# Kernel tuning notes

Hardware: AMD Instinct MI355X
Metric: run time of the kernel (lower is better)

Reference implementation:

```python
import jax, jax.numpy as jnp
import numpy as np

B, S, D = 2, 2048, 2048
H, KVH, HD = 16, 8, 128          # heads, kv heads, head_dim
KVR = 512                        # kv_lora_rank
THETA, ROPE_FACTOR = 10000.0, 40.0
EPS = 1e-5
NEG = -1e9


def _layernorm(x, scale):
    mean = jnp.mean(x, axis=-1, keepdims=True)
    var = jnp.mean(jnp.square(x - mean), axis=-1, keepdims=True)
    return (x - mean) * jax.lax.rsqrt(var + EPS) * scale


def _rope_cos_sin(position_ids):
    # freqs over half the head dim, scaled by rope_factor (as in source)
    freqs = (1.0 / THETA ** (jnp.arange(0, HD, 2, dtype=jnp.float32) / HD)) * ROPE_FACTOR
    ang = position_ids.astype(jnp.float32)[:, None] * freqs[None, :]  # [S, HD//2]
    return jnp.cos(ang)[None, :, None, :], jnp.sin(ang)[None, :, None, :]


def _apply_rope(x, cos, sin):
    # x: [B,S,h,HD] with interleaved (real, imag) pairs
    x_ = x.reshape(*x.shape[:-1], -1, 2)
    xr, xi = x_[..., 0], x_[..., 1]
    out = jnp.stack([xr * cos - xi * sin, xr * sin + xi * cos], axis=-1)
    return out.reshape(x.shape)


def setup_inputs() -> dict:
    key = jax.random.key(0)
    ks = jax.random.split(key, 6)
    std = 0.02
    x = jax.random.normal(ks[0], (B, S, D), jnp.float32)
    wq = jax.random.normal(ks[1], (D, H * 2 * HD), jnp.float32) * std
    wkv_a = jax.random.normal(ks[2], (D, KVR + HD), jnp.float32) * std
    kv_norm_scale = jnp.ones((KVR,), jnp.float32)
    wkv_b = jax.random.normal(ks[3], (KVR, KVH * 2 * HD), jnp.float32) * std
    wo = jax.random.normal(ks[4], (H * HD, D), jnp.float32) * std
    causal = jnp.tril(jnp.ones((S, S), bool))
    attention_mask = jnp.where(causal, 0.0, NEG)[None, None].astype(jnp.float32)
    position_ids = jnp.arange(S, dtype=jnp.int32)
    return {"x": x, "wq": wq, "wkv_a": wkv_a, "kv_norm_scale": kv_norm_scale,
            "wkv_b": wkv_b, "wo": wo, "attention_mask": attention_mask,
            "position_ids": position_ids}


def reference(x, wq, wkv_a, kv_norm_scale, wkv_b, wo, attention_mask, position_ids):
    cos, sin = _rope_cos_sin(position_ids)
    # Q path: low-rank disabled (q_lora_rank=0) -> single projection
    q = (x @ wq).reshape(B, S, H, 2 * HD)
    q_nope, q_pe = q[..., :HD], q[..., HD:]
    q = jnp.concatenate([q_nope, _apply_rope(q_pe, cos, sin)], axis=-1)  # [B,S,H,2HD]
    # KV path: low-rank compression + decoupled rope key
    kv = x @ wkv_a                               # [B,S,KVR+HD]
    kv_c = _layernorm(kv[..., :KVR], kv_norm_scale)
    k_pe = kv[..., KVR:]                         # [B,S,HD]
    kvb = (kv_c @ wkv_b).reshape(B, S, KVH, 2 * HD)
    k_nope, v = kvb[..., :HD], kvb[..., HD:]
    k_pe = _apply_rope(k_pe[:, :, None, :], cos, sin)  # [B,S,1,HD]
    k = jnp.concatenate([k_nope, jnp.broadcast_to(k_pe, (B, S, KVH, HD))], axis=-1)
    # GQA expansion
    rep = H // KVH
    k = jnp.repeat(k, rep, axis=2)
    v = jnp.repeat(v, rep, axis=2)
    scale = HD ** -0.5
    scores = jnp.einsum('bqhd,bkhd->bhqk', q, k) * scale + attention_mask
    probs = jax.nn.softmax(scores, axis=-1)
    attn = jnp.einsum('bhqk,bkhd->bqhd', probs, v).reshape(B, S, H * HD)
    return attn @ wo
```

## Files before the change

### kernel.cpp

```cpp
#include <hip/hip_runtime.h>


typedef __attribute__((ext_vector_type(8))) short short8;
typedef __attribute__((ext_vector_type(4))) float floatx4;
typedef unsigned short u16;
typedef unsigned int u32;

__device__ __forceinline__ float bf2f(u16 u){ u32 x=((u32)u)<<16; return __builtin_bit_cast(float,x); }
__device__ __forceinline__ u16 f2bf(float f){ u32 x=__builtin_bit_cast(u32,f); return (u16)((x + 0x7fffu + ((x>>16)&1u))>>16); }

__device__ __forceinline__ floatx4 mfma16(short8 a, short8 b, floatx4 c){
  return __builtin_amdgcn_mfma_f32_16x16x32_bf16(a,b,c,0,0,0);
}

__device__ __forceinline__ void gl_lds16(const u16* g, u16* l){
  __builtin_amdgcn_global_load_lds((const __attribute__((address_space(1))) void*)g,
                                   (__attribute__((address_space(3))) void*)l, 16, 0, 0);
}

__global__ __launch_bounds__(256)
void k_f2b(const float* __restrict__ in, u16* __restrict__ out, size_t n){
  size_t i = ((size_t)blockIdx.x*256 + threadIdx.x)*4;
  if(i >= n) return;
  float4 v = *(const float4*)(in + i);
  out[i+0] = f2bf(v.x); out[i+1] = f2bf(v.y); out[i+2] = f2bf(v.z); out[i+3] = f2bf(v.w);
}

__global__ void k_transpose(const float* __restrict__ in, u16* __restrict__ out, int K, int N){
  __shared__ u16 tile[32][33];
  const int kb = blockIdx.y*32, nb = blockIdx.x*32;
  const int tx = threadIdx.x, ty = threadIdx.y;
#pragma unroll
  for(int i=0;i<4;i++) tile[ty+i*8][tx] = f2bf(in[(size_t)(kb+ty+i*8)*N + nb + tx]);
  __syncthreads();
#pragma unroll
  for(int i=0;i<4;i++) out[(size_t)(nb+ty+i*8)*K + kb + tx] = tile[tx][ty+i*8];
}

__global__ void k_rope_table(float* __restrict__ cosT, float* __restrict__ sinT){
  int idx = blockIdx.x*256 + threadIdx.x;
  if(idx >= 2048*64) return;
  int p = idx>>6, i = idx&63;
  double freq = pow(10000.0, -(double)(2*i)/128.0) * 40.0;
  float ff = (float)freq;
  float ang = (float)((double)p * (double)ff);
  cosT[idx] = (float)cos((double)ang);
  sinT[idx] = (float)sin((double)ang);
}

template<int OUTF32>
__global__ __launch_bounds__(256)
void k_gemm_bt(const u16* __restrict__ A, const u16* __restrict__ Bt, void* __restrict__ Cout,
               int M, int N, int K){
  __shared__ __align__(16) u16 lsA[128*32];
  __shared__ __align__(16) u16 lsB[128*32];
  const int t = threadIdx.x;
  const int m0 = blockIdx.y*128, n0 = blockIdx.x*128;
  const int wv = t>>6, ln = t&63;
  const int wr = (wv>>1)*64, wc = (wv&1)*64;
  const int fr = ln&15, kh = (ln>>4)*8;
  const int srow = wv*16 + (ln>>2), sk = (ln&3)*8;
  const u16* Ag = A + (size_t)(m0 + srow)*K + sk;
  const u16* Bg = Bt + (size_t)(n0 + srow)*K + sk;
  u16* lA0 = &lsA[wv*512];
  u16* lB0 = &lsB[wv*512];
  floatx4 acc[4][4];
#pragma unroll
  for(int i=0;i<4;i++)
#pragma unroll
    for(int j=0;j<4;j++) acc[i][j] = (floatx4){0.f,0.f,0.f,0.f};
  for(int k0=0;k0<K;k0+=32){
    __syncthreads();
    gl_lds16(Ag + k0,              lA0);
    gl_lds16(Ag + (size_t)64*K + k0, lA0 + 2048);
    gl_lds16(Bg + k0,              lB0);
    gl_lds16(Bg + (size_t)64*K + k0, lB0 + 2048);
    __syncthreads();
    short8 af[4], bf[4];
#pragma unroll
    for(int i=0;i<4;i++) af[i] = *(const short8*)&lsA[(wr + i*16 + fr)*32 + kh];
#pragma unroll
    for(int i=0;i<4;i++) bf[i] = *(const short8*)&lsB[(wc + i*16 + fr)*32 + kh];
#pragma unroll
    for(int mi=0;mi<4;mi++)
#pragma unroll
      for(int ni=0;ni<4;ni++) acc[mi][ni] = mfma16(af[mi], bf[ni], acc[mi][ni]);
  }
  const int r0 = (ln>>4)*4, c0 = ln&15;
#pragma unroll
  for(int mi=0;mi<4;mi++)
#pragma unroll
    for(int ni=0;ni<4;ni++){
      const int row = m0 + wr + mi*16 + r0;
      const int col = n0 + wc + ni*16 + c0;
#pragma unroll
      for(int r=0;r<4;r++){
        float v = acc[mi][ni][r];
        if(OUTF32) ((float*)Cout)[(size_t)(row+r)*N + col] = v;
        else       ((u16*)Cout)[(size_t)(row+r)*N + col] = f2bf(v);
      }
    }
}

__global__ __launch_bounds__(256)
void k_ln_rope(const float* __restrict__ kv, const float* __restrict__ scale,
               const int* __restrict__ pid, const float* __restrict__ cosT,
               const float* __restrict__ sinT, u16* __restrict__ kv_cn, u16* __restrict__ k_pe){
  const int tok = blockIdx.x;
  const int t = threadIdx.x;
  const float* row = kv + (size_t)tok*640;
  float v0 = row[2*t], v1 = row[2*t+1];
  float s = v0+v1, ss = v0*v0+v1*v1;
#pragma unroll
  for(int off=32; off>=1; off>>=1){ s += __shfl_xor(s,off); ss += __shfl_xor(ss,off); }
  __shared__ float red[8];
  if((t&63)==0){ red[t>>6]=s; red[4+(t>>6)]=ss; }
  __syncthreads();
  float S4 = red[0]+red[1]+red[2]+red[3];
  float SS4 = red[4]+red[5]+red[6]+red[7];
  float mean = S4*(1.f/512.f);
  float var = SS4*(1.f/512.f) - mean*mean;
  float inv = rsqrtf(var + 1e-5f);
  kv_cn[(size_t)tok*512 + 2*t]   = f2bf((v0-mean)*inv*scale[2*t]);
  kv_cn[(size_t)tok*512 + 2*t+1] = f2bf((v1-mean)*inv*scale[2*t+1]);
  if(t < 128){
    const int sidx = tok & 2047;
    const int p = pid[sidx];
    const int i = t>>1;
    float c = cosT[p*64+i], sn = sinT[p*64+i];
    float xr = row[512+2*i], xi = row[512+2*i+1];
    float val = (t&1) ? (xr*sn + xi*c) : (xr*c - xi*sn);
    k_pe[(size_t)tok*128 + t] = f2bf(val);
  }
}

__global__ __launch_bounds__(256)
void k_q_rope(const u16* __restrict__ q_raw, const int* __restrict__ pid,
              const float* __restrict__ cosT, const float* __restrict__ sinT,
              u16* __restrict__ q_fin){
  const float QS = (float)(0.08838834764831845 * 1.4426950408889634);
  const int tok = blockIdx.x;
  const int b = tok>>11, sidx = tok&2047;
  const int t = threadIdx.x;
  const int p = pid[sidx];
  const int h = t>>4, seg = t&15;
  const u16* src = q_raw + (size_t)tok*4096 + h*256 + seg*16;
  u16* dst = q_fin + (((size_t)(b*16 + h))*2048 + sidx)*256 + seg*16;
  short8 a = *(const short8*)src;
  short8 bv = *(const short8*)(src+8);
  short8 oa, ob;
  if(seg < 8){
#pragma unroll
    for(int j=0;j<8;j++){
      oa[j] = (short)f2bf(bf2f((u16)a[j])*QS);
      ob[j] = (short)f2bf(bf2f((u16)bv[j])*QS);
    }
  } else {
    const int i0 = seg*8 - 64;
#pragma unroll
    for(int j=0;j<4;j++){
      float c = cosT[p*64 + i0 + j], sn = sinT[p*64 + i0 + j];
      float xr = bf2f((u16)a[2*j]), xi = bf2f((u16)a[2*j+1]);
      oa[2*j]   = (short)f2bf((xr*c - xi*sn)*QS);
      oa[2*j+1] = (short)f2bf((xr*sn + xi*c)*QS);
    }
#pragma unroll
    for(int j=0;j<4;j++){
      float c = cosT[p*64 + i0 + 4 + j], sn = sinT[p*64 + i0 + 4 + j];
      float xr = bf2f((u16)bv[2*j]), xi = bf2f((u16)bv[2*j+1]);
      ob[2*j]   = (short)f2bf((xr*c - xi*sn)*QS);
      ob[2*j+1] = (short)f2bf((xr*sn + xi*c)*QS);
    }
  }
  *(short8*)dst = oa;
  *(short8*)(dst+8) = ob;
}

__global__ __launch_bounds__(256)
void k_build_k(const u16* __restrict__ kvb, const u16* __restrict__ k_pe, u16* __restrict__ k_full){
  const int tok = blockIdx.x;
  const int b = tok>>11, sidx = tok&2047;
  const int t = threadIdx.x;
  const int kh = t>>5, seg = t&31;
  short8 v;
  if(seg < 16) v = *(const short8*)(kvb + (size_t)tok*2048 + kh*256 + seg*8);
  else         v = *(const short8*)(k_pe + (size_t)tok*128 + (seg-16)*8);
  *(short8*)(k_full + (((size_t)(b*8 + kh))*2048 + sidx)*256 + seg*8) = v;
}

__global__ void k_v_t(const u16* __restrict__ kvb, u16* __restrict__ v_t){
  __shared__ u16 tile[32][33];
  const int sb = blockIdx.x*32, hb = blockIdx.y*32;
  const int bk = blockIdx.z;
  const int b = bk>>3, kh = bk&7;
  const int tx = threadIdx.x, ty = threadIdx.y;
#pragma unroll
  for(int i=0;i<4;i++){
    int sidx = sb + ty + i*8;
    tile[ty+i*8][tx] = kvb[((size_t)(b*2048 + sidx))*2048 + kh*256 + 128 + hb + tx];
  }
  __syncthreads();
#pragma unroll
  for(int i=0;i<4;i++){
    int hd = hb + ty + i*8;
    v_t[(((size_t)bk*64 + blockIdx.x)*128 + hd)*32 + tx] = tile[tx][ty+i*8];
  }
}

__global__ __launch_bounds__(256)
void k_attn(const u16* __restrict__ q_fin, const u16* __restrict__ k_full,
            const u16* __restrict__ v_t, u16* __restrict__ attn){
  __shared__ __align__(16) u16 lsK[2*8192];
  __shared__ __align__(16) u16 lsV[2*128*40];
  __shared__ __align__(16) u16 lsP[4*16*40];
  const int blk = blockIdx.x;
  const int g  = (blk>>8)*8 + (blk&7);
  const int i  = (blk>>3)&31;
  const int b  = g>>3, kvh = g&7;
  const int pr = i&15;
  const int h  = kvh*2 + (i>>4);
  const int t = threadIdx.x, wv = t>>6, ln = t&63;
  const int fq = ln&15, gq = ln>>4;
  const u16* kbase = k_full + ((size_t)(b*8 + kvh))*2048*256;
  const u16* vbase = v_t + ((size_t)(b*8 + kvh))*128*2048;
  u16* Pw = &lsP[wv*16*40];

  int soff[4];
#pragma unroll
  for(int s4=0;s4<4;s4++){
    int o = s4*4096 + wv*1024 + ln*16;
    int row = o>>9, colb = o&511;
    soff[s4] = row*512 + (colb ^ ((row&7)<<4));
  }
  const int swz = (fq&7)<<4;
  int cb[8];
#pragma unroll
  for(int c=0;c<8;c++) cb[c] = (gq*16 + c*64) ^ swz;
  const int rowb = fq*512;
  const int vrow = t>>1, vcol = (t&1)*16;

  for(int half=0; half<2; half++){
    const int qt = half ? (31-pr) : pr;
    const int last = 2*qt + 1;
    short8 qf[8];
    const u16* qb = q_fin + (((size_t)(b*16 + h))*2048 + qt*64 + wv*16 + fq)*256;
#pragma unroll
    for(int c=0;c<8;c++) qf[c] = *(const short8*)(qb + c*32 + gq*8);
    floatx4 oacc[8];
#pragma unroll
    for(int ii=0;ii<8;ii++) oacc[ii] = (floatx4){0.f,0.f,0.f,0.f};
    float mprev = -3e38f, lsum = 0.f;

#pragma unroll
    for(int s4=0;s4<4;s4++)
      gl_lds16((const u16*)((const char*)kbase + soff[s4]), &lsK[s4*2048 + wv*512]);
    {
      const u16* vg = vbase + (size_t)t*16;
      short8 v0 = *(const short8*)vg;
      short8 v1 = *(const short8*)(vg+8);
      *(short8*)&lsV[vrow*40 + vcol]     = v0;
      *(short8*)&lsV[vrow*40 + vcol + 8] = v1;
    }
    __syncthreads();

    int cur = 0;
    for(int kt=0; kt<=last; kt++){
      short8 vr0, vr1;
      if(kt < last){
        const char* ktile = (const char*)kbase + (size_t)(kt+1)*16384;
        u16* kdst = &lsK[(cur^1)*8192];
#pragma unroll
        for(int s4=0;s4<4;s4++)
          gl_lds16((const u16*)(ktile + soff[s4]), kdst + s4*2048 + wv*512);
        const u16* vg = vbase + (size_t)(kt+1)*4096 + t*16;
        vr0 = *(const short8*)vg;
        vr1 = *(const short8*)(vg+8);
      }
      const char* Kc = (const char*)lsK + cur*16384;
      const u16* Vc = &lsV[cur*5120];

      floatx4 sc[2];
#pragma unroll
      for(int ns=0;ns<2;ns++) sc[ns] = (floatx4){0.f,0.f,0.f,0.f};
#pragma unroll
      for(int ns=0;ns<2;ns++){
#pragma unroll
        for(int c=0;c<8;c++){
          short8 kf = *(const short8*)(Kc + ns*8192 + rowb + cb[c]);
          sc[ns] = mfma16(kf, qf[c], sc[ns]);
        }
      }
      if(kt >= 2*qt){
        const int off = (kt - 2*qt)*32;
        const int qloc = wv*16 + fq;
#pragma unroll
        for(int ns=0;ns<2;ns++)
#pragma unroll
          for(int r=0;r<4;r++)
            if(off + ns*16 + gq*4 + r > qloc) sc[ns][r] = -1e30f;
      }
      float mloc = -3e38f;
#pragma unroll
      for(int ns=0;ns<2;ns++)
#pragma unroll
        for(int r=0;r<4;r++) mloc = fmaxf(mloc, sc[ns][r]);
      mloc = fmaxf(mloc, __shfl_xor(mloc, 16));
      mloc = fmaxf(mloc, __shfl_xor(mloc, 32));
      const float mn = fmaxf(mprev, mloc);
      const float alpha = exp2f(mprev - mn);
      float ps = 0.f;
#pragma unroll
      for(int ns=0;ns<2;ns++)
#pragma unroll
        for(int r=0;r<4;r++){
          float p = exp2f(sc[ns][r] - mn);
          sc[ns][r] = p;
          ps += p;
        }
      ps += __shfl_xor(ps, 16);
      ps += __shfl_xor(ps, 32);
      lsum = lsum*alpha + ps;
      mprev = mn;

#pragma unroll
      for(int ns=0;ns<2;ns++){
        u32 p01 = (u32)f2bf(sc[ns][0]) | ((u32)f2bf(sc[ns][1])<<16);
        u32 p23 = (u32)f2bf(sc[ns][2]) | ((u32)f2bf(sc[ns][3])<<16);
        uint2 pk; pk.x = p01; pk.y = p23;
        *(uint2*)&Pw[fq*40 + ns*16 + gq*4] = pk;
      }
      float alphaO[4];
#pragma unroll
      for(int r=0;r<4;r++) alphaO[r] = __shfl(alpha, gq*4 + r);
#pragma unroll
      for(int hs=0;hs<8;hs++)
#pragma unroll
        for(int r=0;r<4;r++) oacc[hs][r] *= alphaO[r];
      __builtin_amdgcn_s_waitcnt(0xC07F);

      short8 pa = *(const short8*)&Pw[fq*40 + gq*8];
#pragma unroll
      for(int hs=0;hs<8;hs++){
        short8 vb = *(const short8*)&Vc[(hs*16 + fq)*40 + gq*8];
        oacc[hs] = mfma16(pa, vb, oacc[hs]);
      }
      if(kt < last){
        u16* vd = &lsV[(cur^1)*5120 + vrow*40 + vcol];
        *(short8*)vd     = vr0;
        *(short8*)(vd+8) = vr1;
      }
      __syncthreads();
      cur ^= 1;
    }
    const float inv = 1.f / lsum;
    float invO[4];
#pragma unroll
    for(int r=0;r<4;r++) invO[r] = __shfl(inv, gq*4 + r);
#pragma unroll
    for(int hs=0;hs<8;hs++)
#pragma unroll
      for(int r=0;r<4;r++){
        const int qi = qt*64 + wv*16 + gq*4 + r;
        attn[(((size_t)(b*2048 + qi))*16 + h)*128 + hs*16 + fq] = f2bf(oacc[hs][r]*invO[r]);
      }
  }
}

extern "C" void kernel_launch(void* const* d_in, const int* in_sizes, int n_in,
                              void* d_out, int out_size, void* d_ws, size_t ws_size,
                              hipStream_t stream){
  const float* x    = (const float*)d_in[0];
  const float* wq   = (const float*)d_in[1];
  const float* wkva = (const float*)d_in[2];
  const float* kvsc = (const float*)d_in[3];
  const float* wkvb = (const float*)d_in[4];
  const float* wo   = (const float*)d_in[5];
  const int* pid  = (const int*)d_in[7];
  float* out = (float*)d_out;

  char* w = (char*)d_ws;
  size_t off = 0;
  auto alloc = [&](size_t bytes)->void*{
    void* p = (void*)(w + off);
    off += (bytes + 255) & ~(size_t)255;
    return p;
  };
  u16*   x_bf   = (u16*)alloc((size_t)4096*2048*2);
  u16*   wq_t   = (u16*)alloc((size_t)4096*2048*2);
  u16*   wkva_t = (u16*)alloc((size_t)640*2048*2);
  u16*   wkvb_t = (u16*)alloc((size_t)2048*512*2);
  u16*   wo_t   = (u16*)alloc((size_t)2048*2048*2);
  float* cosT   = (float*)alloc((size_t)2048*64*4);
  float* sinT   = (float*)alloc((size_t)2048*64*4);
  u16*   q_raw  = (u16*)alloc((size_t)4096*4096*2);
  float* kvf    = (float*)alloc((size_t)4096*640*4);
  u16*   kv_cn  = (u16*)alloc((size_t)4096*512*2);
  u16*   k_pe   = (u16*)alloc((size_t)4096*128*2);
  u16*   kvb    = (u16*)alloc((size_t)4096*2048*2);
  u16*   q_fin  = (u16*)alloc((size_t)4096*4096*2);
  u16*   k_full = (u16*)alloc((size_t)2*8*2048*256*2);
  u16*   v_t    = (u16*)alloc((size_t)2*8*128*2048*2);
  u16*   attn   = (u16*)alloc((size_t)4096*2048*2);

  k_f2b<<<8192, 256, 0, stream>>>(x, x_bf, (size_t)4096*2048);
  k_transpose<<<dim3(128, 64), dim3(32,8), 0, stream>>>(wq,   wq_t,   2048, 4096);
  k_transpose<<<dim3(20,  64), dim3(32,8), 0, stream>>>(wkva, wkva_t, 2048, 640);
  k_transpose<<<dim3(64,  16), dim3(32,8), 0, stream>>>(wkvb, wkvb_t, 512,  2048);
  k_transpose<<<dim3(64,  64), dim3(32,8), 0, stream>>>(wo,   wo_t,   2048, 2048);
  k_rope_table<<<512, 256, 0, stream>>>(cosT, sinT);

  k_gemm_bt<0><<<dim3(32, 32), 256, 0, stream>>>(x_bf, wq_t, q_raw, 4096, 4096, 2048);
  k_gemm_bt<1><<<dim3(5,  32), 256, 0, stream>>>(x_bf, wkva_t, kvf, 4096, 640, 2048);
  k_ln_rope<<<4096, 256, 0, stream>>>(kvf, kvsc, pid, cosT, sinT, kv_cn, k_pe);
  k_gemm_bt<0><<<dim3(16, 32), 256, 0, stream>>>(kv_cn, wkvb_t, kvb, 4096, 2048, 512);
  k_q_rope<<<4096, 256, 0, stream>>>(q_raw, pid, cosT, sinT, q_fin);
  k_build_k<<<4096, 256, 0, stream>>>(kvb, k_pe, k_full);
  k_v_t<<<dim3(64, 4, 16), dim3(32,8), 0, stream>>>(kvb, v_t);
  k_attn<<<512, 256, 0, stream>>>(q_fin, k_full, v_t, attn);
  k_gemm_bt<1><<<dim3(16, 32), 256, 0, stream>>>(attn, wo_t, out, 4096, 2048, 2048);
}
```

Before: 525.7 us.

## Split attention into one q-tile per block, load V direct to registers, lazy rescale

The attention kernel now launches one block per query tile (1024 blocks ordered heaviest first) instead of pairing two causal halves per block. V fragments are read straight from global memory into registers rather than staged through double-buffered LDS. The online-softmax rescale is skipped unless the running max grows by more than 8, and bf16 packing uses v_cvt_pk_bf16_f32. These changes aim to cut LDS use and per-tile softmax work and to raise occupancy (launch bounds 3), at the cost of uncoalesced global V loads and load imbalance from the longest-first ordering.

```diff
diff --git a/kernel.cpp b/kernel.cpp
--- a/kernel.cpp
+++ b/kernel.cpp
@@ -207,22 +207,21 @@
   }
 }
 
-__global__ __launch_bounds__(256)
+__global__ __launch_bounds__(256, 3)
 void k_attn(const u16* __restrict__ q_fin, const u16* __restrict__ k_full,
             const u16* __restrict__ v_t, u16* __restrict__ attn){
   __shared__ __align__(16) u16 lsK[2*8192];
-  __shared__ __align__(16) u16 lsV[2*128*40];
   __shared__ __align__(16) u16 lsP[4*16*40];
   const int blk = blockIdx.x;
-  const int g  = (blk>>8)*8 + (blk&7);
-  const int i  = (blk>>3)&31;
-  const int b  = g>>3, kvh = g&7;
-  const int pr = i&15;
-  const int h  = kvh*2 + (i>>4);
+  const int kvh = blk&7;
+  const int bb  = (blk>>3)&1;
+  const int qr  = blk>>4;
+  const int qt  = 31 - (qr>>1);
+  const int h   = kvh*2 + (qr&1);
   const int t = threadIdx.x, wv = t>>6, ln = t&63;
   const int fq = ln&15, gq = ln>>4;
-  const u16* kbase = k_full + ((size_t)(b*8 + kvh))*2048*256;
-  const u16* vbase = v_t + ((size_t)(b*8 + kvh))*128*2048;
+  const u16* kbase = k_full + ((size_t)(bb*8 + kvh))*2048*256;
+  const u16* vbase = v_t + ((size_t)(bb*8 + kvh))*128*2048;
   u16* Pw = &lsP[wv*16*40];
 
   int soff[4];
@@ -237,133 +236,120 @@
 #pragma unroll
   for(int c=0;c<8;c++) cb[c] = (gq*16 + c*64) ^ swz;
   const int rowb = fq*512;
-  const int vrow = t>>1, vcol = (t&1)*16;
-
-  for(int half=0; half<2; half++){
-    const int qt = half ? (31-pr) : pr;
-    const int last = 2*qt + 1;
-    short8 qf[8];
-    const u16* qb = q_fin + (((size_t)(b*16 + h))*2048 + qt*64 + wv*16 + fq)*256;
-#pragma unroll
-    for(int c=0;c<8;c++) qf[c] = *(const short8*)(qb + c*32 + gq*8);
-    floatx4 oacc[8];
-#pragma unroll
-    for(int ii=0;ii<8;ii++) oacc[ii] = (floatx4){0.f,0.f,0.f,0.f};
-    float mprev = -3e38f, lsum = 0.f;
-
-#pragma unroll
-    for(int s4=0;s4<4;s4++)
-      gl_lds16((const u16*)((const char*)kbase + soff[s4]), &lsK[s4*2048 + wv*512]);
-    {
-      const u16* vg = vbase + (size_t)t*16;
-      short8 v0 = *(const short8*)vg;
-      short8 v1 = *(const short8*)(vg+8);
-      *(short8*)&lsV[vrow*40 + vcol]     = v0;
-      *(short8*)&lsV[vrow*40 + vcol + 8] = v1;
-    }
-    __syncthreads();
-
-    int cur = 0;
-    for(int kt=0; kt<=last; kt++){
-      short8 vr0, vr1;
-      if(kt < last){
-        const char* ktile = (const char*)kbase + (size_t)(kt+1)*16384;
-        u16* kdst = &lsK[(cur^1)*8192];
-#pragma unroll
-        for(int s4=0;s4<4;s4++)
-          gl_lds16((const u16*)(ktile + soff[s4]), kdst + s4*2048 + wv*512);
-        const u16* vg = vbase + (size_t)(kt+1)*4096 + t*16;
-        vr0 = *(const short8*)vg;
-        vr1 = *(const short8*)(vg+8);
+  const u16* vfp = vbase + (size_t)fq*32 + gq*8;
+
+  const int last = 2*qt + 1;
+  short8 qf[8];
+  const u16* qb = q_fin + (((size_t)(bb*16 + h))*2048 + qt*64 + wv*16 + fq)*256;
+#pragma unroll
+  for(int c=0;c<8;c++) qf[c] = *(const short8*)(qb + c*32 + gq*8);
+  floatx4 oacc[8];
+#pragma unroll
+  for(int ii=0;ii<8;ii++) oacc[ii] = (floatx4){0.f,0.f,0.f,0.f};
+  float mprev = -3e38f, lsum = 0.f;
+
+#pragma unroll
+  for(int s4=0;s4<4;s4++)
+    gl_lds16((const u16*)((const char*)kbase + soff[s4]), &lsK[s4*2048 + wv*512]);
+  __syncthreads();
+
+  int cur = 0;
+  for(int kt=0; kt<=last; kt++){
+    if(kt < last){
+      const char* ktile = (const char*)kbase + (size_t)(kt+1)*16384;
+      u16* kdst = &lsK[(cur^1)*8192];
+#pragma unroll
+      for(int s4=0;s4<4;s4++)
+        gl_lds16((const u16*)(ktile + soff[s4]), kdst + s4*2048 + wv*512);
+    }
+    short8 vf[8];
+#pragma unroll
+    for(int hs=0;hs<8;hs++)
+      vf[hs] = *(const short8*)(vfp + (size_t)kt*4096 + hs*512);
+
+    const char* Kc = (const char*)lsK + cur*16384;
+    floatx4 sc[2];
+#pragma unroll
+    for(int ns=0;ns<2;ns++) sc[ns] = (floatx4){0.f,0.f,0.f,0.f};
+#pragma unroll
+    for(int ns=0;ns<2;ns++){
+#pragma unroll
+      for(int c=0;c<8;c++){
+        short8 kf = *(const short8*)(Kc + ns*8192 + rowb + cb[c]);
+        sc[ns] = mfma16(kf, qf[c], sc[ns]);
       }
-      const char* Kc = (const char*)lsK + cur*16384;
-      const u16* Vc = &lsV[cur*5120];
-
-      floatx4 sc[2];
-#pragma unroll
-      for(int ns=0;ns<2;ns++) sc[ns] = (floatx4){0.f,0.f,0.f,0.f};
-#pragma unroll
-      for(int ns=0;ns<2;ns++){
-#pragma unroll
-        for(int c=0;c<8;c++){
-          short8 kf = *(const short8*)(Kc + ns*8192 + rowb + cb[c]);
-          sc[ns] = mfma16(kf, qf[c], sc[ns]);
-        }
-      }
-      if(kt >= 2*qt){
-        const int off = (kt - 2*qt)*32;
-        const int qloc = wv*16 + fq;
-#pragma unroll
-        for(int ns=0;ns<2;ns++)
-#pragma unroll
-          for(int r=0;r<4;r++)
-            if(off + ns*16 + gq*4 + r > qloc) sc[ns][r] = -1e30f;
-      }
-      float mloc = -3e38f;
+    }
+    if(kt >= 2*qt){
+      const int off = (kt - 2*qt)*32;
+      const int qloc = wv*16 + fq;
 #pragma unroll
       for(int ns=0;ns<2;ns++)
 #pragma unroll
-        for(int r=0;r<4;r++) mloc = fmaxf(mloc, sc[ns][r]);
-      mloc = fmaxf(mloc, __shfl_xor(mloc, 16));
-      mloc = fmaxf(mloc, __shfl_xor(mloc, 32));
+        for(int r=0;r<4;r++)
+          if(off + ns*16 + gq*4 + r > qloc) sc[ns][r] = -1e30f;
+    }
+    float mloc = -3e38f;
+#pragma unroll
+    for(int ns=0;ns<2;ns++)
+#pragma unroll
+      for(int r=0;r<4;r++) mloc = fmaxf(mloc, sc[ns][r]);
+    mloc = fmaxf(mloc, __shfl_xor(mloc, 16));
+    mloc = fmaxf(mloc, __shfl_xor(mloc, 32));
+    if(__any(mloc > mprev + 8.f)){
       const float mn = fmaxf(mprev, mloc);
       const float alpha = exp2f(mprev - mn);
-      float ps = 0.f;
-#pragma unroll
-      for(int ns=0;ns<2;ns++)
-#pragma unroll
-        for(int r=0;r<4;r++){
-          float p = exp2f(sc[ns][r] - mn);
-          sc[ns][r] = p;
-          ps += p;
-        }
-      ps += __shfl_xor(ps, 16);
-      ps += __shfl_xor(ps, 32);
-      lsum = lsum*alpha + ps;
+      lsum *= alpha;
+      float alphaO[4];
+#pragma unroll
+      for(int r=0;r<4;r++) alphaO[r] = __shfl(alpha, gq*4 + r);
+#pragma unroll
+      for(int hs=0;hs<8;hs++)
+#pragma unroll
+        for(int r=0;r<4;r++) oacc[hs][r] *= alphaO[r];
       mprev = mn;
-
-#pragma unroll
-      for(int ns=0;ns<2;ns++){
-        u32 p01 = (u32)f2bf(sc[ns][0]) | ((u32)f2bf(sc[ns][1])<<16);
-        u32 p23 = (u32)f2bf(sc[ns][2]) | ((u32)f2bf(sc[ns][3])<<16);
-        uint2 pk; pk.x = p01; pk.y = p23;
-        *(uint2*)&Pw[fq*40 + ns*16 + gq*4] = pk;
+    }
+    float ps = 0.f;
+#pragma unroll
+    for(int ns=0;ns<2;ns++)
+#pragma unroll
+      for(int r=0;r<4;r++){
+        float p = exp2f(sc[ns][r] - mprev);
+        sc[ns][r] = p;
+        ps += p;
       }
-      float alphaO[4];
-#pragma unroll
-      for(int r=0;r<4;r++) alphaO[r] = __shfl(alpha, gq*4 + r);
-#pragma unroll
-      for(int hs=0;hs<8;hs++)
-#pragma unroll
-        for(int r=0;r<4;r++) oacc[hs][r] *= alphaO[r];
-      __builtin_amdgcn_s_waitcnt(0xC07F);
-
-      short8 pa = *(const short8*)&Pw[fq*40 + gq*8];
-#pragma unroll
-      for(int hs=0;hs<8;hs++){
-        short8 vb = *(const short8*)&Vc[(hs*16 + fq)*40 + gq*8];
-        oacc[hs] = mfma16(pa, vb, oacc[hs]);
-      }
-      if(kt < last){
-        u16* vd = &lsV[(cur^1)*5120 + vrow*40 + vcol];
-        *(short8*)vd     = vr0;
-        *(short8*)(vd+8) = vr1;
-      }
-      __syncthreads();
-      cur ^= 1;
-    }
-    const float inv = 1.f / lsum;
-    float invO[4];
-#pragma unroll
-    for(int r=0;r<4;r++) invO[r] = __shfl(inv, gq*4 + r);
+    ps += __shfl_xor(ps, 16);
+    ps += __shfl_xor(ps, 32);
+    lsum += ps;
+
+#pragma unroll
+    for(int ns=0;ns<2;ns++){
+      u32 p01, p23;
+      asm("v_cvt_pk_bf16_f32 %0, %1, %2" : "=v"(p01) : "v"(sc[ns][0]), "v"(sc[ns][1]));
+      asm("v_cvt_pk_bf16_f32 %0, %1, %2" : "=v"(p23) : "v"(sc[ns][2]), "v"(sc[ns][3]));
+      uint2 pk; pk.x = p01; pk.y = p23;
+      *(uint2*)&Pw[fq*40 + ns*16 + gq*4] = pk;
+    }
+    __builtin_amdgcn_s_waitcnt(0xC07F);
+
+    short8 pa = *(const short8*)&Pw[fq*40 + gq*8];
 #pragma unroll
     for(int hs=0;hs<8;hs++)
-#pragma unroll
-      for(int r=0;r<4;r++){
-        const int qi = qt*64 + wv*16 + gq*4 + r;
-        attn[(((size_t)(b*2048 + qi))*16 + h)*128 + hs*16 + fq] = f2bf(oacc[hs][r]*invO[r]);
-      }
-  }
+      oacc[hs] = mfma16(pa, vf[hs], oacc[hs]);
+
+    __syncthreads();
+    cur ^= 1;
+  }
+  const float inv = 1.f / lsum;
+  float invO[4];
+#pragma unroll
+  for(int r=0;r<4;r++) invO[r] = __shfl(inv, gq*4 + r);
+#pragma unroll
+  for(int hs=0;hs<8;hs++)
+#pragma unroll
+    for(int r=0;r<4;r++){
+      const int qi = qt*64 + wv*16 + gq*4 + r;
+      attn[(((size_t)(bb*2048 + qi))*16 + h)*128 + hs*16 + fq] = f2bf(oacc[hs][r]*invO[r]);
+    }
 }
 
 extern "C" void kernel_launch(void* const* d_in, const int* in_sizes, int n_in,
@@ -416,6 +402,6 @@
   k_q_rope<<<4096, 256, 0, stream>>>(q_raw, pid, cosT, sinT, q_fin);
   k_build_k<<<4096, 256, 0, stream>>>(kvb, k_pe, k_full);
   k_v_t<<<dim3(64, 4, 16), dim3(32,8), 0, stream>>>(kvb, v_t);
-  k_attn<<<512, 256, 0, stream>>>(q_fin, k_full, v_t, attn);
+  k_attn<<<1024, 256, 0, stream>>>(q_fin, k_full, v_t, attn);
   k_gemm_bt<1><<<dim3(16, 32), 256, 0, stream>>>(attn, wo_t, out, 4096, 2048, 2048);
 }
```

Result: no change. 517.9 us (-1.5%).
